# Performance work log

Hardware: AMD Instinct MI355X
Metric: run time of the kernel (lower is better)

Reference implementation:

```python
import jax, jax.numpy as jnp
import numpy as np

B, G, D = 8192, 32, 64
N_USERS, N_ITEMS, N_GROUPS = 200000, 50000, 20000
CLS_BIAS = 0.5


def setup_inputs() -> dict:
    key = jax.random.key(0)
    ks = jax.random.split(key, 16)
    s = lambda k, shape: (jax.random.normal(k, shape, dtype=jnp.float32) * 0.05)
    return {
        'group_inputs': jax.random.randint(ks[0], (B,), 0, N_GROUPS),
        'item_inputs': jax.random.randint(ks[1], (B,), 0, N_ITEMS),
        'members': jax.random.randint(ks[2], (B, G), 0, N_USERS),
        'user_table': s(ks[3], (N_USERS, D)),
        'item_table': s(ks[4], (N_ITEMS, D)),
        'group_table': s(ks[5], (N_GROUPS, D)),
        'group_embedds': s(ks[6], (N_GROUPS, D)),
        'att_w1': s(ks[7], (2 * D, 16)), 'att_b1': jnp.zeros((16,), jnp.float32),
        'att_w2': s(ks[8], (16, 1)), 'att_b2': jnp.zeros((1,), jnp.float32),
        'cls_w': s(ks[9], (1, 2)), 'cls_b': jnp.zeros((2,), jnp.float32),
        'pred_w1': s(ks[10], (3 * D, 8)), 'pred_b1': jnp.zeros((8,), jnp.float32),
        'pred_w2': s(ks[11], (8, 1)), 'pred_b2': jnp.zeros((1,), jnp.float32),
    }


def reference(group_inputs, item_inputs, members, user_table, item_table,
              group_table, group_embedds, att_w1, att_b1, att_w2, att_b2,
              cls_w, cls_b, pred_w1, pred_b1, pred_w2, pred_b2):
    # gather member / item embeddings (irregular access hot path)
    mem_emb = user_table[members]                      # [B, G, D]
    item_emb = item_table[item_inputs]                 # [B, D]
    gi = jnp.concatenate(
        [mem_emb, jnp.broadcast_to(item_emb[:, None, :], mem_emb.shape)], axis=-1)  # [B, G, 2D]
    # AttentionLayer(2D): Linear -> ReLU -> Linear(->1) -> softmax over members
    h = jax.nn.relu(jnp.einsum('bgc,ch->bgh', gi, att_w1) + att_b1)
    scores = (jnp.einsum('bgh,ho->bgo', h, att_w2) + att_b2)[..., 0]  # [B, G]
    at_wt = jax.nn.softmax(scores, axis=-1)            # [B, G]
    # routing branch: classifier on the max attention weight
    max_idx = jnp.argmax(at_wt, axis=-1)               # [B]
    max_w = jnp.max(at_wt, axis=-1, keepdims=True)     # [B, 1]
    cls_scores = max_w @ cls_w + cls_b                 # [B, 2]
    cls_scores = cls_scores.at[:, 1].add(CLS_BIAS)
    pred_cls = jnp.argmax(jax.nn.softmax(cls_scores, axis=-1), axis=-1)  # [B]
    leader_emb = jnp.take_along_axis(mem_emb, max_idx[:, None, None], axis=1)[:, 0]  # [B, D]
    weighted_emb = jnp.einsum('bg,bgd->bd', at_wt, mem_emb)
    g_att = jnp.where((pred_cls == 1)[:, None], leader_emb, weighted_emb)
    # pure group embedding + precomputed group embeds
    g_pure = group_table[group_inputs] + group_embedds[group_inputs]
    g = g_att + g_pure                                 # [B, D]
    # PredictLayer(3D): Linear -> ReLU -> Linear -> sigmoid
    elem = g * item_emb
    new_embeds = jnp.concatenate([elem, g, item_emb], axis=-1)  # [B, 3D]
    ph = jax.nn.relu(new_embeds @ pred_w1 + pred_b1)
    y = jax.nn.sigmoid(ph @ pred_w2 + pred_b2)         # [B, 1]
    return new_embeds, y, at_wt, pred_cls
```

## Files before the change

kernel.cpp:

```cpp
#include <hip/hip_runtime.h>

#define BB 8192
#define GG 32
#define DD 64

#define QUAD_XOR1 0xB1
#define QUAD_XOR2 0x4E
#define ROW_ROR4  0x124
#define ROW_ROR8  0x128

template<int CTRL>
__device__ __forceinline__ float dpp_mov(float x) {
    return __int_as_float(__builtin_amdgcn_update_dpp(
        __float_as_int(x), __float_as_int(x), CTRL, 0xF, 0xF, false));
}
__device__ __forceinline__ float row16_sum(float x) {
    x += dpp_mov<QUAD_XOR1>(x);
    x += dpp_mov<QUAD_XOR2>(x);
    x += dpp_mov<ROW_ROR4>(x);
    x += dpp_mov<ROW_ROR8>(x);
    return x;
}
__device__ __forceinline__ float row16_max(float x) {
    x = fmaxf(x, dpp_mov<QUAD_XOR1>(x));
    x = fmaxf(x, dpp_mov<QUAD_XOR2>(x));
    x = fmaxf(x, dpp_mov<ROW_ROR4>(x));
    x = fmaxf(x, dpp_mov<ROW_ROR8>(x));
    return x;
}
template<int CTRL>
__device__ __forceinline__ int dpp_mov_i(int x) {
    return __builtin_amdgcn_update_dpp(x, x, CTRL, 0xF, 0xF, false);
}
__device__ __forceinline__ int row16_min_i(int x) {
    x = min(x, dpp_mov_i<QUAD_XOR1>(x));
    x = min(x, dpp_mov_i<QUAD_XOR2>(x));
    x = min(x, dpp_mov_i<ROW_ROR4>(x));
    x = min(x, dpp_mov_i<ROW_ROR8>(x));
    return x;
}
__device__ __forceinline__ float half_sum(float x) { x = row16_sum(x); return x + __shfl_xor(x, 16); }
__device__ __forceinline__ float half_max(float x) { x = row16_max(x); return fmaxf(x, __shfl_xor(x, 16)); }
__device__ __forceinline__ int   half_min_i(int x) { x = row16_min_i(x); return min(x, __shfl_xor(x, 16)); }

__global__ __launch_bounds__(256)
void hhgr_kernel(const int* __restrict__ group_inputs,
                 const int* __restrict__ item_inputs,
                 const int* __restrict__ members,
                 const float* __restrict__ user_table,
                 const float* __restrict__ item_table,
                 const float* __restrict__ group_table,
                 const float* __restrict__ group_embedds,
                 const float* __restrict__ att_w1, const float* __restrict__ att_b1,
                 const float* __restrict__ att_w2, const float* __restrict__ att_b2,
                 const float* __restrict__ cls_w, const float* __restrict__ cls_b,
                 const float* __restrict__ pred_w1, const float* __restrict__ pred_b1,
                 const float* __restrict__ pred_w2, const float* __restrict__ pred_b2,
                 float* __restrict__ out)
{
    __shared__ float awt_s[8][32];
    __shared__ int   midx_s[8][32];

    const int tid  = threadIdx.x;
    const int m    = tid & 31;
    const int slot = tid >> 5;
    const int wl   = tid & 63;
    const int hw   = wl >> 5;
    const int b    = blockIdx.x * 8 + slot;

    const int midx = members[b * GG + m];
    const int iidx = item_inputs[b];
    const int gidx = group_inputs[b];

    float4 mr[16];
    {
        const float4* urow = (const float4*)(user_table + (size_t)midx * DD);
#pragma unroll
        for (int i = 0; i < 16; ++i) mr[i] = urow[i];
    }

    float h[16];
    {
        const float2 it2 = *(const float2*)(item_table + (size_t)iidx * DD + 2 * m);
        const float4* wa = (const float4*)(att_w1 + (64 + 2 * m) * 16);
        const float4* wb = (const float4*)(att_w1 + (65 + 2 * m) * 16);
#pragma unroll
        for (int q4 = 0; q4 < 4; ++q4) {
            const float4 a  = wa[q4];
            const float4 bq = wb[q4];
            h[4 * q4 + 0] = fmaf(it2.y, bq.x, it2.x * a.x);
            h[4 * q4 + 1] = fmaf(it2.y, bq.y, it2.x * a.y);
            h[4 * q4 + 2] = fmaf(it2.y, bq.z, it2.x * a.z);
            h[4 * q4 + 3] = fmaf(it2.y, bq.w, it2.x * a.w);
        }
#pragma unroll
        for (int i = 0; i < 16; ++i)
            h[i] = half_sum(h[i]) + att_b1[i];
    }

#pragma unroll
    for (int i = 0; i < 16; ++i) {
#pragma unroll
        for (int j = 0; j < 4; ++j) {
            const float mk = (j == 0) ? mr[i].x : (j == 1) ? mr[i].y
                           : (j == 2) ? mr[i].z : mr[i].w;
            const float* wr = att_w1 + (4 * i + j) * 16;
#pragma unroll
            for (int oo = 0; oo < 16; ++oo)
                h[oo] = fmaf(mk, wr[oo], h[oo]);
        }
    }

    float sc = att_b2[0];
#pragma unroll
    for (int oo = 0; oo < 16; ++oo)
        sc = fmaf(fmaxf(h[oo], 0.f), att_w2[oo], sc);

    const float smax = half_max(sc);
    const float e    = expf(sc - smax);
    const float ssum = half_sum(e);
    const float w    = e / ssum;
    out[(size_t)BB * 193 + (size_t)b * GG + m] = w;

    const float wmax = half_max(w);
    const int   idx  = half_min_i((w == wmax) ? m : 1000);

    const float cs0 = fmaf(wmax, cls_w[0], cls_b[0]);
    const float cs1 = fmaf(wmax, cls_w[1], cls_b[1]) + 0.5f;
    const int pred  = (cs1 > cs0) ? 1 : 0;

    float gA, gB;
    if (pred) {
        const int lmidx = __shfl(midx, hw * 32 + idx);
        const float* lrow = user_table + (size_t)lmidx * DD;
        gA = lrow[m];
        gB = lrow[m + 32];
    } else {
        awt_s[slot][m]  = w;
        midx_s[slot][m] = midx;
        __builtin_amdgcn_s_waitcnt(0);
        float accA = 0.f, accB = 0.f;
        for (int g = 0; g < GG; ++g) {
            const float wg = awt_s[slot][g];
            const float* grow = user_table + (size_t)midx_s[slot][g] * DD;
            accA = fmaf(wg, grow[m], accA);
            accB = fmaf(wg, grow[m + 32], accB);
        }
        gA = accA; gB = accB;
    }

    const float gpA = group_table[(size_t)gidx * DD + m]      + group_embedds[(size_t)gidx * DD + m];
    const float gpB = group_table[(size_t)gidx * DD + m + 32] + group_embedds[(size_t)gidx * DD + m + 32];
    const float itA = item_table[(size_t)iidx * DD + m];
    const float itB = item_table[(size_t)iidx * DD + m + 32];
    const float gvA = gA + gpA, gvB = gB + gpB;
    const float elA = gvA * itA, elB = gvB * itB;

    const size_t nb = (size_t)b * 192;
    out[nb + m]        = elA;  out[nb + 32 + m]  = elB;
    out[nb + 64 + m]   = gvA;  out[nb + 96 + m]  = gvB;
    out[nb + 128 + m]  = itA;  out[nb + 160 + m] = itB;

    float p8[8];
#pragma unroll
    for (int j = 0; j < 8; ++j) p8[j] = 0.f;

    {
        const float vals[6] = { elA, elB, gvA, gvB, itA, itB };
        const int   cols[6] = { m, m + 32, 64 + m, 96 + m, 128 + m, 160 + m };
#pragma unroll
        for (int t = 0; t < 6; ++t) {
            const float4* wr = (const float4*)(pred_w1 + cols[t] * 8);
            const float4 w0 = wr[0], w1v = wr[1];
            p8[0] = fmaf(vals[t], w0.x, p8[0]);
            p8[1] = fmaf(vals[t], w0.y, p8[1]);
            p8[2] = fmaf(vals[t], w0.z, p8[2]);
            p8[3] = fmaf(vals[t], w0.w, p8[3]);
            p8[4] = fmaf(vals[t], w1v.x, p8[4]);
            p8[5] = fmaf(vals[t], w1v.y, p8[5]);
            p8[6] = fmaf(vals[t], w1v.z, p8[6]);
            p8[7] = fmaf(vals[t], w1v.w, p8[7]);
        }
    }
#pragma unroll
    for (int j = 0; j < 8; ++j)
        p8[j] = half_sum(p8[j]) + pred_b1[j];

    float t2 = pred_b2[0];
#pragma unroll
    for (int j = 0; j < 8; ++j)
        t2 = fmaf(fmaxf(p8[j], 0.f), pred_w2[j], t2);
    const float yv = 1.f / (1.f + expf(-t2));

    if (m == 0) {
        out[(size_t)BB * 192 + b] = yv;
        out[(size_t)BB * 225 + b] = (float)pred;
    }
}

extern "C" void kernel_launch(void* const* d_in, const int* in_sizes, int n_in,
                              void* d_out, int out_size, void* d_ws, size_t ws_size,
                              hipStream_t stream) {
    const int*   group_inputs  = (const int*)d_in[0];
    const int*   item_inputs   = (const int*)d_in[1];
    const int*   members       = (const int*)d_in[2];
    const float* user_table    = (const float*)d_in[3];
    const float* item_table    = (const float*)d_in[4];
    const float* group_table   = (const float*)d_in[5];
    const float* group_embedds = (const float*)d_in[6];
    const float* att_w1  = (const float*)d_in[7];
    const float* att_b1  = (const float*)d_in[8];
    const float* att_w2  = (const float*)d_in[9];
    const float* att_b2  = (const float*)d_in[10];
    const float* cls_w   = (const float*)d_in[11];
    const float* cls_b   = (const float*)d_in[12];
    const float* pred_w1 = (const float*)d_in[13];
    const float* pred_b1 = (const float*)d_in[14];
    const float* pred_w2 = (const float*)d_in[15];
    const float* pred_b2 = (const float*)d_in[16];
    float* out = (float*)d_out;

    hipLaunchKernelGGL(hhgr_kernel, dim3(BB / 8), dim3(256), 0, stream,
                       group_inputs, item_inputs, members, user_table, item_table,
                       group_table, group_embedds, att_w1, att_b1, att_w2, att_b2,
                       cls_w, cls_b, pred_w1, pred_b1, pred_w2, pred_b2, out);
}
```

Before: 144.8 us.

## Stream member rows in chunks, add occupancy hint, derive max weight from softmax sum

Stops holding the full 64-float member row in registers and streams it in four chunks of four float4s, prefetching the next chunk while the current one is consumed. The launch bound now requests four blocks per CU. This is meant to cut VGPR pressure and raise occupancy for this latency-bound gather kernel. The item-embedding slice per lane changes from an interleaved float2 to two strided scalars so the loads coalesce. The max attention weight is now computed as 1/sum and the argmax from raw scores, which removes a cross-lane max reduction but may differ from the reference by rounding at ties.

```diff
diff --git a/kernel.cpp b/kernel.cpp
--- a/kernel.cpp
+++ b/kernel.cpp
@@ -43,7 +43,7 @@
 __device__ __forceinline__ float half_max(float x) { x = row16_max(x); return fmaxf(x, __shfl_xor(x, 16)); }
 __device__ __forceinline__ int   half_min_i(int x) { x = row16_min_i(x); return min(x, __shfl_xor(x, 16)); }
 
-__global__ __launch_bounds__(256)
+__global__ __launch_bounds__(256, 4)
 void hhgr_kernel(const int* __restrict__ group_inputs,
                  const int* __restrict__ item_inputs,
                  const int* __restrict__ members,
@@ -72,43 +72,47 @@
     const int iidx = item_inputs[b];
     const int gidx = group_inputs[b];
 
-    float4 mr[16];
-    {
-        const float4* urow = (const float4*)(user_table + (size_t)midx * DD);
-#pragma unroll
-        for (int i = 0; i < 16; ++i) mr[i] = urow[i];
-    }
+    const float* urowp = user_table + (size_t)midx * DD;
+    const float4* urow = (const float4*)urowp;
+
+    const float itx = item_table[(size_t)iidx * DD + m];
+    const float ity = item_table[(size_t)iidx * DD + 32 + m];
+    const float4* wa = (const float4*)(att_w1 + (64 + m) * 16);
+    const float4* wb = (const float4*)(att_w1 + (96 + m) * 16);
+
+    float4 buf0 = urow[0], buf1 = urow[1], buf2 = urow[2], buf3 = urow[3];
 
     float h[16];
-    {
-        const float2 it2 = *(const float2*)(item_table + (size_t)iidx * DD + 2 * m);
-        const float4* wa = (const float4*)(att_w1 + (64 + 2 * m) * 16);
-        const float4* wb = (const float4*)(att_w1 + (65 + 2 * m) * 16);
-#pragma unroll
-        for (int q4 = 0; q4 < 4; ++q4) {
-            const float4 a  = wa[q4];
-            const float4 bq = wb[q4];
-            h[4 * q4 + 0] = fmaf(it2.y, bq.x, it2.x * a.x);
-            h[4 * q4 + 1] = fmaf(it2.y, bq.y, it2.x * a.y);
-            h[4 * q4 + 2] = fmaf(it2.y, bq.z, it2.x * a.z);
-            h[4 * q4 + 3] = fmaf(it2.y, bq.w, it2.x * a.w);
+#pragma unroll
+    for (int q4 = 0; q4 < 4; ++q4) {
+        const float4 a  = wa[q4];
+        const float4 bq = wb[q4];
+        h[4 * q4 + 0] = fmaf(ity, bq.x, itx * a.x);
+        h[4 * q4 + 1] = fmaf(ity, bq.y, itx * a.y);
+        h[4 * q4 + 2] = fmaf(ity, bq.z, itx * a.z);
+        h[4 * q4 + 3] = fmaf(ity, bq.w, itx * a.w);
+    }
+#pragma unroll
+    for (int i = 0; i < 16; ++i)
+        h[i] = half_sum(h[i]) + att_b1[i];
+
+#pragma unroll
+    for (int q = 0; q < 4; ++q) {
+        float4 n0, n1, n2, n3;
+        if (q < 3) { n0 = urow[4*q+4]; n1 = urow[4*q+5]; n2 = urow[4*q+6]; n3 = urow[4*q+7]; }
+#pragma unroll
+        for (int kk = 0; kk < 4; ++kk) {
+            const float4 v = (kk == 0) ? buf0 : (kk == 1) ? buf1 : (kk == 2) ? buf2 : buf3;
+            const float* wr = att_w1 + (16 * q + 4 * kk) * 16;
+#pragma unroll
+            for (int oo = 0; oo < 16; ++oo) {
+                h[oo] = fmaf(v.x, wr[oo],      h[oo]);
+                h[oo] = fmaf(v.y, wr[16 + oo], h[oo]);
+                h[oo] = fmaf(v.z, wr[32 + oo], h[oo]);
+                h[oo] = fmaf(v.w, wr[48 + oo], h[oo]);
+            }
         }
-#pragma unroll
-        for (int i = 0; i < 16; ++i)
-            h[i] = half_sum(h[i]) + att_b1[i];
-    }
-
-#pragma unroll
-    for (int i = 0; i < 16; ++i) {
-#pragma unroll
-        for (int j = 0; j < 4; ++j) {
-            const float mk = (j == 0) ? mr[i].x : (j == 1) ? mr[i].y
-                           : (j == 2) ? mr[i].z : mr[i].w;
-            const float* wr = att_w1 + (4 * i + j) * 16;
-#pragma unroll
-            for (int oo = 0; oo < 16; ++oo)
-                h[oo] = fmaf(mk, wr[oo], h[oo]);
-        }
+        if (q < 3) { buf0 = n0; buf1 = n1; buf2 = n2; buf3 = n3; }
     }
 
     float sc = att_b2[0];
@@ -122,8 +126,8 @@
     const float w    = e / ssum;
     out[(size_t)BB * 193 + (size_t)b * GG + m] = w;
 
-    const float wmax = half_max(w);
-    const int   idx  = half_min_i((w == wmax) ? m : 1000);
+    const float wmax = 1.0f / ssum;
+    const int   idx  = half_min_i((sc == smax) ? m : 1000);
 
     const float cs0 = fmaf(wmax, cls_w[0], cls_b[0]);
     const float cs1 = fmaf(wmax, cls_w[1], cls_b[1]) + 0.5f;
@@ -164,7 +168,6 @@
     float p8[8];
 #pragma unroll
     for (int j = 0; j < 8; ++j) p8[j] = 0.f;
-
     {
         const float vals[6] = { elA, elB, gvA, gvB, itA, itB };
         const int   cols[6] = { m, m + 32, 64 + m, 96 + m, 128 + m, 160 + m };
```

Measured after the change: 147.4 us. Within noise of the previous version (+1.8%).
